# Performance work log

Measured on AMD Instinct MI355X. Metric: run time of the kernel, lower is better.

## Reference

```python
import jax, jax.numpy as jnp
import numpy as np

B, S, E, H = 4, 2048, 1024, 16
D = E // H
EPS = 1e-6


def setup_inputs() -> dict:
    key = jax.random.key(0)
    ks = jax.random.split(key, 6)
    glorot = lambda k: jax.random.uniform(k, (E, E), jnp.float32,
                                          -np.sqrt(6.0 / (E + E)), np.sqrt(6.0 / (E + E)))
    return {
        "x": jax.random.normal(ks[0], (B, S, E), jnp.float32),
        "mask": jnp.zeros((B, 1, 1, S), jnp.float32),
        "Wq": glorot(ks[1]), "bq": jnp.zeros((E,), jnp.float32),
        "Wk": glorot(ks[2]), "bk": jnp.zeros((E,), jnp.float32),
        "Wv": glorot(ks[3]), "bv": jnp.zeros((E,), jnp.float32),
        "Wo": glorot(ks[4]), "bo": jnp.zeros((E,), jnp.float32),
        "gamma": jnp.ones((E,), jnp.float32),
        "beta": jnp.zeros((E,), jnp.float32),
    }


def _split_heads(t):
    # [B, S, E] -> [B, H, S, D]
    return t.reshape(B, S, H, D).transpose(0, 2, 1, 3)


def reference(x, mask, Wq, bq, Wk, bk, Wv, bv, Wo, bo, gamma, beta):
    q = _split_heads(x @ Wq + bq)
    k = _split_heads(x @ Wk + bk)
    v = _split_heads(x @ Wv + bv)
    # NOTE: original divides by sqrt(embedding_size), not sqrt(depth)
    scores = jnp.einsum("bhqd,bhkd->bhqk", q, k) / jnp.sqrt(jnp.float32(E))
    scores = scores + mask * (-1e9)
    attn = jax.nn.softmax(scores, axis=-1)
    ctx = jnp.einsum("bhqk,bhkd->bhqd", attn, v)
    ctx = ctx.transpose(0, 2, 1, 3).reshape(B, S, E)
    main_out = ctx @ Wo + bo
    # dropout is identity (is_training=False); residual is the raw input
    added = main_out + x
    mu = jnp.mean(added, axis=-1, keepdims=True)
    var = jnp.mean(jnp.square(added - mu), axis=-1, keepdims=True)
    return gamma * (added - mu) / jnp.sqrt(var + EPS) + beta
```

## Files before the change

kernel.cpp:

```cpp
#include <hip/hip_runtime.h>
#include <hip/hip_bf16.h>


typedef __bf16 bf16_t;
typedef __bf16 bf16x8 __attribute__((ext_vector_type(8)));
typedef __bf16 bf16x4v __attribute__((ext_vector_type(4)));
typedef float f32x4 __attribute__((ext_vector_type(4)));

#define LDS_AS __attribute__((address_space(3)))
#define GLB_AS __attribute__((address_space(1)))

__device__ __forceinline__ void async16(bf16_t* lds, const bf16_t* g) {
  __builtin_amdgcn_global_load_lds((GLB_AS void*)const_cast<bf16_t*>(g),
                                   (LDS_AS void*)lds, 16, 0, 0);
}

__device__ __forceinline__ f32x4 mfma16(bf16x8 a, bf16x8 b, f32x4 c) {
  return __builtin_amdgcn_mfma_f32_16x16x32_bf16(a, b, c, 0, 0, 0);
}

__device__ __forceinline__ float fast_exp2(float x) {
#if __has_builtin(__builtin_amdgcn_exp2f)
  return __builtin_amdgcn_exp2f(x);
#else
  return __expf(x * 0.6931471805599453f);
#endif
}

__global__ __launch_bounds__(256) void prep_k(
    const float* __restrict__ w0, const float* __restrict__ w1,
    const float* __restrict__ w2, const float* __restrict__ w3,
    bf16_t* __restrict__ dst,
    const float* __restrict__ x, bf16_t* __restrict__ xb)
{
  const int tx = threadIdx.x, ty = threadIdx.y;
  if (blockIdx.z == 4) {
    const int id = (blockIdx.y * 32 + blockIdx.x) * 256 + ty * 32 + tx;
#pragma unroll
    for (int it = 0; it < 8; ++it) {
      const size_t i = ((size_t)id + (size_t)it * 262144) * 4;
      const float4 v = *(const float4*)(x + i);
      bf16x4v o;
      o[0] = (bf16_t)v.x; o[1] = (bf16_t)v.y; o[2] = (bf16_t)v.z; o[3] = (bf16_t)v.w;
      *(bf16x4v*)(xb + i) = o;
    }
    return;
  }
  __shared__ bf16_t tile[32][33];
  const float* src = (blockIdx.z == 0) ? w0 : (blockIdx.z == 1) ? w1
                   : (blockIdx.z == 2) ? w2 : w3;
  bf16_t* d = dst + (size_t)blockIdx.z * 1024 * 1024;
  const int bx = blockIdx.x * 32, by = blockIdx.y * 32;
#pragma unroll
  for (int r = 0; r < 32; r += 8)
    tile[ty + r][tx] = (bf16_t)src[(size_t)(by + ty + r) * 1024 + bx + tx];
  __syncthreads();
#pragma unroll
  for (int r = 0; r < 32; r += 8)
    d[(size_t)(bx + ty + r) * 1024 + by + tx] = tile[tx][ty + r];
}

__global__ __launch_bounds__(256) void gemm_qkv(
    const bf16_t* __restrict__ X, const bf16_t* __restrict__ WtAll,
    const float* __restrict__ bq, const float* __restrict__ bk,
    const float* __restrict__ bv,
    bf16_t* __restrict__ Qb, bf16_t* __restrict__ Kb, bf16_t* __restrict__ Vtb)
{
  __shared__ __align__(16) bf16_t As[128 * 64];
  __shared__ __align__(16) bf16_t Bs[128 * 64];

  const int z = blockIdx.z;
  const bf16_t* Bt = WtAll + (size_t)z * 1024 * 1024;
  const float* bias = (z == 0) ? bq : (z == 1) ? bk : bv;
  const int bm0 = blockIdx.x * 128;
  const int bn0 = blockIdx.y * 128;
  const int t = threadIdx.x;
  const int w = t >> 6, lane = t & 63;
  const int wm = w >> 1, wn = w & 1;
  const int l15 = lane & 15, quad = lane >> 4;
  const int srow8 = lane >> 3;
  const int sp8   = lane & 7;

  f32x4 acc[4][4] = {};

  for (int k0 = 0; k0 < 1024; k0 += 64) {
    __syncthreads();
#pragma unroll
    for (int i = 0; i < 4; ++i) {
      const int row = (w * 4 + i) * 8 + srow8;
      const int c = sp8 ^ (row & 7);
      async16(&As[row * 64 + sp8 * 8], X  + (size_t)(bm0 + row) * 1024 + k0 + c * 8);
      async16(&Bs[row * 64 + sp8 * 8], Bt + (size_t)(bn0 + row) * 1024 + k0 + c * 8);
    }
    __syncthreads();

    bf16x8 af[4][2], bfr[4][2];
#pragma unroll
    for (int mi = 0; mi < 4; ++mi) {
      const int r = wm * 64 + mi * 16 + l15;
#pragma unroll
      for (int kc = 0; kc < 2; ++kc) {
        const int pg = (kc * 4 + quad) ^ (r & 7);
        af[mi][kc] = *(const bf16x8*)&As[r * 64 + pg * 8];
      }
    }
#pragma unroll
    for (int ni = 0; ni < 4; ++ni) {
      const int r = wn * 64 + ni * 16 + l15;
#pragma unroll
      for (int kc = 0; kc < 2; ++kc) {
        const int pg = (kc * 4 + quad) ^ (r & 7);
        bfr[ni][kc] = *(const bf16x8*)&Bs[r * 64 + pg * 8];
      }
    }
#pragma unroll
    for (int kc = 0; kc < 2; ++kc)
#pragma unroll
      for (int mi = 0; mi < 4; ++mi)
#pragma unroll
        for (int ni = 0; ni < 4; ++ni)
          acc[mi][ni] = mfma16(af[mi][kc], bfr[ni][kc], acc[mi][ni]);
  }

  const float QSCALE = 0.045084220f;

#pragma unroll
  for (int ni = 0; ni < 4; ++ni) {
    const int n = bn0 + wn * 64 + ni * 16 + l15;
    const float bb = bias[n];
    const int h = n >> 6, dd = n & 63;
    if (z == 2) {
#pragma unroll
      for (int mi = 0; mi < 4; ++mi) {
        const int m0 = bm0 + wm * 64 + mi * 16 + quad * 4;
        const int bi = m0 >> 11, s = m0 & 2047;
        bf16x4v vk;
#pragma unroll
        for (int r = 0; r < 4; ++r) vk[r] = (bf16_t)(acc[mi][ni][r] + bb);
        *(bf16x4v*)&Vtb[((size_t)(bi * 16 + h) * 64 + dd) * 2048 + s] = vk;
      }
    } else {
#pragma unroll
      for (int mi = 0; mi < 4; ++mi) {
#pragma unroll
        for (int r = 0; r < 4; ++r) {
          const int m = bm0 + wm * 64 + mi * 16 + quad * 4 + r;
          const float v = acc[mi][ni][r] + bb;
          const int bi = m >> 11, s = m & 2047;
          if (z == 0)
            Qb[((size_t)(bi * 16 + h) * 2048 + s) * 64 + dd] = (bf16_t)(v * QSCALE);
          else
            Kb[((size_t)(bi * 16 + h) * 2048 + s) * 64 + dd] = (bf16_t)v;
        }
      }
    }
  }
}

__global__ __launch_bounds__(256) void attn_k(
    const bf16_t* __restrict__ Qb, const bf16_t* __restrict__ Kb,
    const bf16_t* __restrict__ Vtb, const float* __restrict__ mask,
    bf16_t* __restrict__ Ctx)
{
  __shared__ __align__(16) bf16_t Ks[64 * 64];
  __shared__ __align__(16) bf16_t Vs[64 * 64];
  __shared__ __align__(16) bf16_t Ps[256 * 64];
  __shared__ __align__(16) float maskv[64];

  const int qt = blockIdx.x, bh = blockIdx.y;
  const int bi = bh >> 4, h = bh & 15;
  const int q0 = qt * 256;
  const bf16_t* Qh = Qb + (size_t)bh * 2048 * 64;
  const bf16_t* Kh = Kb + (size_t)bh * 2048 * 64;
  const bf16_t* Vh = Vtb + (size_t)bh * 64 * 2048;

  const int t = threadIdx.x;
  const int w = t >> 6, lane = t & 63;
  const int l15 = lane & 15, quad = lane >> 4;

  bf16x8 qb[4][2];
#pragma unroll
  for (int ni = 0; ni < 4; ++ni)
#pragma unroll
    for (int kc = 0; kc < 2; ++kc)
      qb[ni][kc] = *(const bf16x8*)&Qh[(size_t)(q0 + w * 64 + ni * 16 + l15) * 64
                                       + kc * 32 + quad * 8];

  bf16x8 ones;
#pragma unroll
  for (int i = 0; i < 8; ++i) ones[i] = (bf16_t)1.0f;

  f32x4 oacc[4][4] = {};
  f32x4 lacc[4] = {};

  const int srow = lane >> 3;
  const int sp = lane & 7;

  for (int j = 0; j < 32; ++j) {
    const int k0 = j * 64;
    __syncthreads();
#pragma unroll
    for (int i = 0; i < 2; ++i) {
      const int row = (w * 2 + i) * 8 + srow;
      const int c = sp ^ (row & 7);
      async16(&Ks[row * 64 + sp * 8], Kh + (size_t)(k0 + row) * 64 + c * 8);
      async16(&Vs[row * 64 + sp * 8], Vh + (size_t)row * 2048 + k0 + c * 8);
    }
    if (t < 64) maskv[t] = mask[bi * 2048 + k0 + t] * (-1.442695e9f);
    __syncthreads();

    f32x4 sacc[4][4];
#pragma unroll
    for (int mi = 0; mi < 4; ++mi) {
      const float4 mk = *(const float4*)&maskv[mi * 16 + quad * 4];
      f32x4 cinit; cinit[0] = mk.x; cinit[1] = mk.y; cinit[2] = mk.z; cinit[3] = mk.w;
#pragma unroll
      for (int ni = 0; ni < 4; ++ni) sacc[mi][ni] = cinit;
    }
#pragma unroll
    for (int mi = 0; mi < 4; ++mi) {
      const int r = mi * 16 + l15;
      const bf16x8 kf0 = *(const bf16x8*)&Ks[r * 64 + ((0 * 4 + quad) ^ (r & 7)) * 8];
      const bf16x8 kf1 = *(const bf16x8*)&Ks[r * 64 + ((1 * 4 + quad) ^ (r & 7)) * 8];
#pragma unroll
      for (int ni = 0; ni < 4; ++ni) {
        sacc[mi][ni] = mfma16(kf0, qb[ni][0], sacc[mi][ni]);
        sacc[mi][ni] = mfma16(kf1, qb[ni][1], sacc[mi][ni]);
      }
    }

#pragma unroll
    for (int ni = 0; ni < 4; ++ni) {
      const int row = w * 64 + ni * 16 + l15;
#pragma unroll
      for (int mi = 0; mi < 4; ++mi) {
        bf16x4v pk;
        pk[0] = (bf16_t)fast_exp2(sacc[mi][ni][0]);
        pk[1] = (bf16_t)fast_exp2(sacc[mi][ni][1]);
        pk[2] = (bf16_t)fast_exp2(sacc[mi][ni][2]);
        pk[3] = (bf16_t)fast_exp2(sacc[mi][ni][3]);
        const int pg = (mi * 2 + (quad >> 1)) ^ (row & 7);
        *(bf16x4v*)&Ps[row * 64 + pg * 8 + (quad & 1) * 4] = pk;
      }
    }

    bf16x8 pb[4][2];
#pragma unroll
    for (int ni = 0; ni < 4; ++ni)
#pragma unroll
      for (int kc = 0; kc < 2; ++kc) {
        const int row = w * 64 + ni * 16 + l15;
        const int pg = (kc * 4 + quad) ^ (row & 7);
        pb[ni][kc] = *(const bf16x8*)&Ps[row * 64 + pg * 8];
      }
#pragma unroll
    for (int mi = 0; mi < 4; ++mi) {
      const int r = mi * 16 + l15;
      const bf16x8 av0 = *(const bf16x8*)&Vs[r * 64 + ((0 * 4 + quad) ^ (r & 7)) * 8];
      const bf16x8 av1 = *(const bf16x8*)&Vs[r * 64 + ((1 * 4 + quad) ^ (r & 7)) * 8];
#pragma unroll
      for (int ni = 0; ni < 4; ++ni) {
        oacc[mi][ni] = mfma16(av0, pb[ni][0], oacc[mi][ni]);
        oacc[mi][ni] = mfma16(av1, pb[ni][1], oacc[mi][ni]);
      }
    }
#pragma unroll
    for (int ni = 0; ni < 4; ++ni) {
      lacc[ni] = mfma16(ones, pb[ni][0], lacc[ni]);
      lacc[ni] = mfma16(ones, pb[ni][1], lacc[ni]);
    }
  }

#pragma unroll
  for (int ni = 0; ni < 4; ++ni) {
    const float inv = 1.0f / lacc[ni][0];
    const int s = q0 + w * 64 + ni * 16 + l15;
#pragma unroll
    for (int mi = 0; mi < 4; ++mi) {
      bf16x4v o4;
      o4[0] = (bf16_t)(oacc[mi][ni][0] * inv);
      o4[1] = (bf16_t)(oacc[mi][ni][1] * inv);
      o4[2] = (bf16_t)(oacc[mi][ni][2] * inv);
      o4[3] = (bf16_t)(oacc[mi][ni][3] * inv);
      *(bf16x4v*)&Ctx[((size_t)bi * 2048 + s) * 1024 + h * 64 + mi * 16 + quad * 4] = o4;
    }
  }
}

__global__ __launch_bounds__(256) void gemm_proj(
    const bf16_t* __restrict__ Ctx, const bf16_t* __restrict__ WoT,
    const float* __restrict__ bo, const float* __restrict__ Xres,
    float* __restrict__ Add)
{
  __shared__ __align__(16) bf16_t As[128 * 64];
  __shared__ __align__(16) bf16_t Bs[128 * 64];

  const int bm0 = blockIdx.x * 128;
  const int bn0 = blockIdx.y * 128;
  const int t = threadIdx.x;
  const int w = t >> 6, lane = t & 63;
  const int wm = w >> 1, wn = w & 1;
  const int l15 = lane & 15, quad = lane >> 4;
  const int srow8 = lane >> 3;
  const int sp8   = lane & 7;

  f32x4 acc[4][4] = {};

  for (int k0 = 0; k0 < 1024; k0 += 64) {
    __syncthreads();
#pragma unroll
    for (int i = 0; i < 4; ++i) {
      const int row = (w * 4 + i) * 8 + srow8;
      const int c = sp8 ^ (row & 7);
      async16(&As[row * 64 + sp8 * 8], Ctx + (size_t)(bm0 + row) * 1024 + k0 + c * 8);
      async16(&Bs[row * 64 + sp8 * 8], WoT + (size_t)(bn0 + row) * 1024 + k0 + c * 8);
    }
    __syncthreads();

    bf16x8 af[4][2], bfr[4][2];
#pragma unroll
    for (int mi = 0; mi < 4; ++mi) {
      const int r = wm * 64 + mi * 16 + l15;
#pragma unroll
      for (int kc = 0; kc < 2; ++kc) {
        const int pg = (kc * 4 + quad) ^ (r & 7);
        af[mi][kc] = *(const bf16x8*)&As[r * 64 + pg * 8];
      }
    }
#pragma unroll
    for (int ni = 0; ni < 4; ++ni) {
      const int r = wn * 64 + ni * 16 + l15;
#pragma unroll
      for (int kc = 0; kc < 2; ++kc) {
        const int pg = (kc * 4 + quad) ^ (r & 7);
        bfr[ni][kc] = *(const bf16x8*)&Bs[r * 64 + pg * 8];
      }
    }
#pragma unroll
    for (int kc = 0; kc < 2; ++kc)
#pragma unroll
      for (int mi = 0; mi < 4; ++mi)
#pragma unroll
        for (int ni = 0; ni < 4; ++ni)
          acc[mi][ni] = mfma16(af[mi][kc], bfr[ni][kc], acc[mi][ni]);
  }

#pragma unroll
  for (int ni = 0; ni < 4; ++ni) {
    const int n = bn0 + wn * 64 + ni * 16 + l15;
    const float bb = bo[n];
#pragma unroll
    for (int mi = 0; mi < 4; ++mi) {
#pragma unroll
      for (int r = 0; r < 4; ++r) {
        const int m = bm0 + wm * 64 + mi * 16 + quad * 4 + r;
        Add[(size_t)m * 1024 + n] =
            acc[mi][ni][r] + bb + Xres[(size_t)m * 1024 + n];
      }
    }
  }
}

__global__ __launch_bounds__(256) void ln_k(
    const float* __restrict__ A, const float* __restrict__ gamma,
    const float* __restrict__ beta, float* __restrict__ out)
{
  const int wid = threadIdx.x >> 6, lane = threadIdx.x & 63;
  const int row = blockIdx.x * 4 + wid;
  const float* a = A + (size_t)row * 1024;

  float4 v[4];
#pragma unroll
  for (int k = 0; k < 4; ++k) v[k] = ((const float4*)a)[lane + k * 64];

  float s = 0.f;
#pragma unroll
  for (int k = 0; k < 4; ++k) s += (v[k].x + v[k].y) + (v[k].z + v[k].w);
#pragma unroll
  for (int o = 1; o < 64; o <<= 1) s += __shfl_xor(s, o);
  const float mu = s * (1.0f / 1024.0f);

  float q = 0.f;
#pragma unroll
  for (int k = 0; k < 4; ++k) {
    v[k].x -= mu; v[k].y -= mu; v[k].z -= mu; v[k].w -= mu;
    q += (v[k].x * v[k].x + v[k].y * v[k].y) + (v[k].z * v[k].z + v[k].w * v[k].w);
  }
#pragma unroll
  for (int o = 1; o < 64; o <<= 1) q += __shfl_xor(q, o);
  const float rs = rsqrtf(q * (1.0f / 1024.0f) + 1e-6f);

#pragma unroll
  for (int k = 0; k < 4; ++k) {
    const int c = lane + k * 64;
    const float4 g4 = ((const float4*)gamma)[c];
    const float4 b4 = ((const float4*)beta)[c];
    float4 o4;
    o4.x = g4.x * v[k].x * rs + b4.x;
    o4.y = g4.y * v[k].y * rs + b4.y;
    o4.z = g4.z * v[k].z * rs + b4.z;
    o4.w = g4.w * v[k].w * rs + b4.w;
    ((float4*)(out + (size_t)row * 1024))[c] = o4;
  }
}

extern "C" void kernel_launch(void* const* d_in, const int* in_sizes, int n_in,
                              void* d_out, int out_size, void* d_ws, size_t ws_size,
                              hipStream_t stream)
{
  const float* x     = (const float*)d_in[0];
  const float* mask  = (const float*)d_in[1];
  const float* Wq    = (const float*)d_in[2];
  const float* bq    = (const float*)d_in[3];
  const float* Wk    = (const float*)d_in[4];
  const float* bk    = (const float*)d_in[5];
  const float* Wv    = (const float*)d_in[6];
  const float* bv    = (const float*)d_in[7];
  const float* Wo    = (const float*)d_in[8];
  const float* bo    = (const float*)d_in[9];
  const float* gamma = (const float*)d_in[10];
  const float* beta  = (const float*)d_in[11];
  float* out = (float*)d_out;

  bf16_t* Wt  = (bf16_t*)d_ws;
  bf16_t* Xb  = Wt + (size_t)4 * 1024 * 1024;
  bf16_t* Qb  = Xb + (size_t)8192 * 1024;
  bf16_t* Kb  = Qb + (size_t)8192 * 1024;
  bf16_t* Vtb = Kb + (size_t)8192 * 1024;
  bf16_t* Ctx = Vtb + (size_t)8192 * 1024;
  float*  Add = (float*)(Ctx + (size_t)8192 * 1024);

  prep_k<<<dim3(32, 32, 5), dim3(32, 8), 0, stream>>>(Wq, Wk, Wv, Wo, Wt, x, Xb);
  gemm_qkv<<<dim3(64, 8, 3), 256, 0, stream>>>(Xb, Wt, bq, bk, bv, Qb, Kb, Vtb);
  attn_k<<<dim3(8, 64), 256, 0, stream>>>(Qb, Kb, Vtb, mask, Ctx);
  gemm_proj<<<dim3(64, 8), 256, 0, stream>>>(Ctx, Wt + (size_t)3 * 1024 * 1024, bo, x, Add);
  ln_k<<<2048, 256, 0, stream>>>(Add, gamma, beta, out);
}
```

Before: 300.6 us.

## Double-buffer K/V tiles in attention with async prefetch and one barrier

Splits the K and V shared-memory tiles into two buffers so the async global-to-LDS loads for the next key block are issued while the current block is computed. Each iteration now has a single barrier instead of two. The mask is read straight from global memory rather than staged through LDS. s_setprio is raised around the MFMA sections. The price is extra LDS per block, which may lower occupancy.

```diff
diff --git a/kernel.cpp b/kernel.cpp
--- a/kernel.cpp
+++ b/kernel.cpp
@@ -162,10 +162,9 @@
     const bf16_t* __restrict__ Vtb, const float* __restrict__ mask,
     bf16_t* __restrict__ Ctx)
 {
-  __shared__ __align__(16) bf16_t Ks[64 * 64];
-  __shared__ __align__(16) bf16_t Vs[64 * 64];
+  __shared__ __align__(16) bf16_t Ks[2][64 * 64];
+  __shared__ __align__(16) bf16_t Vs[2][64 * 64];
   __shared__ __align__(16) bf16_t Ps[256 * 64];
-  __shared__ __align__(16) float maskv[64];
 
   const int qt = blockIdx.x, bh = blockIdx.y;
   const int bi = bh >> 4, h = bh & 15;
@@ -173,10 +172,13 @@
   const bf16_t* Qh = Qb + (size_t)bh * 2048 * 64;
   const bf16_t* Kh = Kb + (size_t)bh * 2048 * 64;
   const bf16_t* Vh = Vtb + (size_t)bh * 64 * 2048;
+  const float* mrow = mask + (size_t)bi * 2048;
 
   const int t = threadIdx.x;
   const int w = t >> 6, lane = t & 63;
   const int l15 = lane & 15, quad = lane >> 4;
+  const int srow = lane >> 3;
+  const int sp = lane & 7;
 
   bf16x8 qb[4][2];
 #pragma unroll
@@ -193,83 +195,108 @@
   f32x4 oacc[4][4] = {};
   f32x4 lacc[4] = {};
 
-  const int srow = lane >> 3;
-  const int sp = lane & 7;
-
-  for (int j = 0; j < 32; ++j) {
-    const int k0 = j * 64;
-    __syncthreads();
-#pragma unroll
-    for (int i = 0; i < 2; ++i) {
-      const int row = (w * 2 + i) * 8 + srow;
-      const int c = sp ^ (row & 7);
-      async16(&Ks[row * 64 + sp * 8], Kh + (size_t)(k0 + row) * 64 + c * 8);
-      async16(&Vs[row * 64 + sp * 8], Vh + (size_t)row * 2048 + k0 + c * 8);
-    }
-    if (t < 64) maskv[t] = mask[bi * 2048 + k0 + t] * (-1.442695e9f);
-    __syncthreads();
-
-    f32x4 sacc[4][4];
-#pragma unroll
-    for (int mi = 0; mi < 4; ++mi) {
-      const float4 mk = *(const float4*)&maskv[mi * 16 + quad * 4];
-      f32x4 cinit; cinit[0] = mk.x; cinit[1] = mk.y; cinit[2] = mk.z; cinit[3] = mk.w;
-#pragma unroll
-      for (int ni = 0; ni < 4; ++ni) sacc[mi][ni] = cinit;
-    }
-#pragma unroll
-    for (int mi = 0; mi < 4; ++mi) {
-      const int r = mi * 16 + l15;
-      const bf16x8 kf0 = *(const bf16x8*)&Ks[r * 64 + ((0 * 4 + quad) ^ (r & 7)) * 8];
-      const bf16x8 kf1 = *(const bf16x8*)&Ks[r * 64 + ((1 * 4 + quad) ^ (r & 7)) * 8];
-#pragma unroll
-      for (int ni = 0; ni < 4; ++ni) {
-        sacc[mi][ni] = mfma16(kf0, qb[ni][0], sacc[mi][ni]);
-        sacc[mi][ni] = mfma16(kf1, qb[ni][1], sacc[mi][ni]);
-      }
-    }
-
-#pragma unroll
-    for (int ni = 0; ni < 4; ++ni) {
-      const int row = w * 64 + ni * 16 + l15;
-#pragma unroll
-      for (int mi = 0; mi < 4; ++mi) {
-        bf16x4v pk;
-        pk[0] = (bf16_t)fast_exp2(sacc[mi][ni][0]);
-        pk[1] = (bf16_t)fast_exp2(sacc[mi][ni][1]);
-        pk[2] = (bf16_t)fast_exp2(sacc[mi][ni][2]);
-        pk[3] = (bf16_t)fast_exp2(sacc[mi][ni][3]);
-        const int pg = (mi * 2 + (quad >> 1)) ^ (row & 7);
-        *(bf16x4v*)&Ps[row * 64 + pg * 8 + (quad & 1) * 4] = pk;
-      }
-    }
-
-    bf16x8 pb[4][2];
-#pragma unroll
-    for (int ni = 0; ni < 4; ++ni)
-#pragma unroll
-      for (int kc = 0; kc < 2; ++kc) {
-        const int row = w * 64 + ni * 16 + l15;
-        const int pg = (kc * 4 + quad) ^ (row & 7);
-        pb[ni][kc] = *(const bf16x8*)&Ps[row * 64 + pg * 8];
-      }
-#pragma unroll
-    for (int mi = 0; mi < 4; ++mi) {
-      const int r = mi * 16 + l15;
-      const bf16x8 av0 = *(const bf16x8*)&Vs[r * 64 + ((0 * 4 + quad) ^ (r & 7)) * 8];
-      const bf16x8 av1 = *(const bf16x8*)&Vs[r * 64 + ((1 * 4 + quad) ^ (r & 7)) * 8];
-#pragma unroll
-      for (int ni = 0; ni < 4; ++ni) {
-        oacc[mi][ni] = mfma16(av0, pb[ni][0], oacc[mi][ni]);
-        oacc[mi][ni] = mfma16(av1, pb[ni][1], oacc[mi][ni]);
-      }
-    }
-#pragma unroll
-    for (int ni = 0; ni < 4; ++ni) {
-      lacc[ni] = mfma16(ones, pb[ni][0], lacc[ni]);
-      lacc[ni] = mfma16(ones, pb[ni][1], lacc[ni]);
-    }
-  }
+#pragma unroll
+  for (int i = 0; i < 2; ++i) {
+    const int row = (w * 2 + i) * 8 + srow;
+    const int c = sp ^ (row & 7);
+    async16(&Ks[0][row * 64 + sp * 8], Kh + (size_t)row * 64 + c * 8);
+    async16(&Vs[0][row * 64 + sp * 8], Vh + (size_t)row * 2048 + c * 8);
+  }
+  __syncthreads();
+
+#define ATTN_STEP(J, KC, VC, KN, VN, PREF)                                     \
+  do {                                                                         \
+    const int k0_ = (J) * 64;                                                  \
+    asm volatile("s_waitcnt vmcnt(0)" ::: "memory");                           \
+    __builtin_amdgcn_s_barrier();                                              \
+    asm volatile("" ::: "memory");                                             \
+    if (PREF) {                                                                \
+      const int k1_ = k0_ + 64;                                                \
+      _Pragma("unroll")                                                        \
+      for (int i = 0; i < 2; ++i) {                                            \
+        const int row = (w * 2 + i) * 8 + srow;                                \
+        const int c = sp ^ (row & 7);                                          \
+        async16(&(KN)[row * 64 + sp * 8], Kh + (size_t)(k1_ + row) * 64 + c * 8); \
+        async16(&(VN)[row * 64 + sp * 8], Vh + (size_t)row * 2048 + k1_ + c * 8); \
+      }                                                                        \
+    }                                                                          \
+      \
+    f32x4 sacc[4][4];                                                          \
+    const float4* m4_ = (const float4*)(mrow + k0_);                           \
+    _Pragma("unroll")                                                          \
+    for (int mi = 0; mi < 4; ++mi) {                                           \
+      const float4 mk = m4_[mi * 4 + quad];                                    \
+      f32x4 ci;                                                                \
+      ci[0] = mk.x * (-1.442695e9f);                                           \
+      ci[1] = mk.y * (-1.442695e9f);                                           \
+      ci[2] = mk.z * (-1.442695e9f);                                           \
+      ci[3] = mk.w * (-1.442695e9f);                                           \
+      _Pragma("unroll")                                                        \
+      for (int ni = 0; ni < 4; ++ni) sacc[mi][ni] = ci;                        \
+    }                                                                          \
+    __builtin_amdgcn_s_setprio(1);                                             \
+    _Pragma("unroll")                                                          \
+    for (int mi = 0; mi < 4; ++mi) {                                           \
+      const int r = mi * 16 + l15;                                             \
+      const bf16x8 kf0 = *(const bf16x8*)&(KC)[r * 64 + ((0 * 4 + quad) ^ (r & 7)) * 8]; \
+      const bf16x8 kf1 = *(const bf16x8*)&(KC)[r * 64 + ((1 * 4 + quad) ^ (r & 7)) * 8]; \
+      _Pragma("unroll")                                                        \
+      for (int ni = 0; ni < 4; ++ni) {                                         \
+        sacc[mi][ni] = mfma16(kf0, qb[ni][0], sacc[mi][ni]);                   \
+        sacc[mi][ni] = mfma16(kf1, qb[ni][1], sacc[mi][ni]);                   \
+      }                                                                        \
+    }                                                                          \
+    __builtin_amdgcn_s_setprio(0);                                             \
+                  \
+    _Pragma("unroll")                                                          \
+    for (int ni = 0; ni < 4; ++ni) {                                           \
+      const int row = w * 64 + ni * 16 + l15;                                  \
+      _Pragma("unroll")                                                        \
+      for (int mi = 0; mi < 4; ++mi) {                                         \
+        bf16x4v pk;                                                            \
+        pk[0] = (bf16_t)fast_exp2(sacc[mi][ni][0]);                            \
+        pk[1] = (bf16_t)fast_exp2(sacc[mi][ni][1]);                            \
+        pk[2] = (bf16_t)fast_exp2(sacc[mi][ni][2]);                            \
+        pk[3] = (bf16_t)fast_exp2(sacc[mi][ni][3]);                            \
+        const int pg = (mi * 2 + (quad >> 1)) ^ (row & 7);                     \
+        *(bf16x4v*)&Ps[row * 64 + pg * 8 + (quad & 1) * 4] = pk;               \
+      }                                                                        \
+    }                                                                          \
+                                           \
+    bf16x8 pb[4][2];                                                           \
+    _Pragma("unroll")                                                          \
+    for (int ni = 0; ni < 4; ++ni)                                             \
+      _Pragma("unroll")                                                        \
+      for (int kc = 0; kc < 2; ++kc) {                                         \
+        const int row = w * 64 + ni * 16 + l15;                                \
+        const int pg = (kc * 4 + quad) ^ (row & 7);                            \
+        pb[ni][kc] = *(const bf16x8*)&Ps[row * 64 + pg * 8];                   \
+      }                                                                        \
+    __builtin_amdgcn_s_setprio(1);                                             \
+    _Pragma("unroll")                                                          \
+    for (int mi = 0; mi < 4; ++mi) {                                           \
+      const int r = mi * 16 + l15;                                             \
+      const bf16x8 av0 = *(const bf16x8*)&(VC)[r * 64 + ((0 * 4 + quad) ^ (r & 7)) * 8]; \
+      const bf16x8 av1 = *(const bf16x8*)&(VC)[r * 64 + ((1 * 4 + quad) ^ (r & 7)) * 8]; \
+      _Pragma("unroll")                                                        \
+      for (int ni = 0; ni < 4; ++ni) {                                         \
+        oacc[mi][ni] = mfma16(av0, pb[ni][0], oacc[mi][ni]);                   \
+        oacc[mi][ni] = mfma16(av1, pb[ni][1], oacc[mi][ni]);                   \
+      }                                                                        \
+    }                                                                          \
+    _Pragma("unroll")                                                          \
+    for (int ni = 0; ni < 4; ++ni) {                                           \
+      lacc[ni] = mfma16(ones, pb[ni][0], lacc[ni]);                            \
+      lacc[ni] = mfma16(ones, pb[ni][1], lacc[ni]);                            \
+    }                                                                          \
+    __builtin_amdgcn_s_setprio(0);                                             \
+  } while (0)
+
+  for (int jj = 0; jj < 16; ++jj) {
+    ATTN_STEP(2 * jj,     Ks[0], Vs[0], Ks[1], Vs[1], true);
+    ATTN_STEP(2 * jj + 1, Ks[1], Vs[1], Ks[0], Vs[0], jj < 15);
+  }
+#undef ATTN_STEP
 
 #pragma unroll
   for (int ni = 0; ni < 4; ++ni) {
```

Result: slower. 339.8 us (+13.0%).
